# Performance work log

Measured on AMD Instinct MI355X. Metric: run time of the kernel, lower is better.

Reference implementation:

```python
import jax, jax.numpy as jnp
import numpy as np

DIM = 512
HEADS = 8
DHEAD = 64
INNER = HEADS * DHEAD
CHUNK = 8
GAMMA = 1.0
EPS = 1e-8
LN_EPS = 1e-5


def setup_inputs() -> dict:
    key = jax.random.key(0)
    ks = jax.random.split(key, 10)
    B, N = 64, 256
    return {
        "q": jax.random.normal(ks[0], (B, N, DIM), jnp.float32),
        "k": jax.random.normal(ks[1], (B, N, DIM), jnp.float32),
        "v": jax.random.normal(ks[2], (B, N, DIM), jnp.float32),
        "ln_gamma": jnp.ones((DIM,), jnp.float32),
        "ln_beta": jnp.zeros((DIM,), jnp.float32),
        "W_in": jax.random.normal(ks[3], (DIM, INNER), jnp.float32) / np.sqrt(DIM),
        "W_out": jax.random.normal(ks[4], (INNER, DIM), jnp.float32) / np.sqrt(INNER),
        "b_out": jnp.zeros((DIM,), jnp.float32),
        "cov_logit": jnp.asarray(0.6, jnp.float32),
        "var_logit": jnp.asarray(0.2, jnp.float32),
        "use_advanced": 1,
    }


def _layernorm(x, g, b):
    mu = jnp.mean(x, axis=-1, keepdims=True)
    var = jnp.mean(jnp.square(x - mu), axis=-1, keepdims=True)
    return (x - mu) * jax.lax.rsqrt(var + LN_EPS) * g + b


def _transform(t, ln_gamma, ln_beta, W_in):
    # [B,N,dim] -> [h,B,N,d]
    B, N, _ = t.shape
    f = _layernorm(t, ln_gamma, ln_beta) @ W_in
    return f.reshape(B, N, HEADS, DHEAD).transpose(2, 0, 1, 3)


def _chunk_stats(E):
    # E: [M, N, d], chunks of size CHUNK over M. Returns per-chunk scalars V, C of shape [M//CHUNK].
    M, N, d = E.shape
    nc = M // CHUNK
    Ec = E.reshape(nc, CHUNK, N, d)
    # variance component: torch.var is unbiased (ddof=1) over seq dim
    sigma = jnp.sqrt(jnp.var(Ec, axis=2, ddof=1) + EPS)  # [nc, CHUNK, d]
    V = jnp.mean(jax.nn.relu(GAMMA - sigma), axis=(1, 2))  # [nc]
    # covariance component: per-sample off-diagonal energy, averaged per chunk
    centered = Ec - jnp.mean(Ec, axis=2, keepdims=True)
    cov = jnp.einsum("csni,csnj->csij", centered, centered) / (N - 1)  # [nc,CHUNK,d,d]
    total = jnp.sum(jnp.square(cov), axis=(2, 3))
    diag = jnp.sum(jnp.square(jnp.diagonal(cov, axis1=2, axis2=3)), axis=2)
    C = jnp.mean((total - diag) / d, axis=1)  # [nc]
    return V, C


def reference(q, k, v, ln_gamma, ln_beta, W_in, W_out, b_out, cov_logit, var_logit, use_advanced):
    f_q = _transform(q, ln_gamma, ln_beta, W_in)  # [h,B,N,d]
    f_k = _transform(k, ln_gamma, ln_beta, W_in)
    f_v = _transform(v, ln_gamma, ln_beta, W_in)
    h, B, N, d = f_q.shape

    # cosine similarity
    dots_qk = jnp.einsum("hbnd,hbmd->hbnm", f_q, f_k)
    qn = jnp.linalg.norm(f_q, axis=-1)  # [h,B,N]
    kn = jnp.linalg.norm(f_k, axis=-1)
    cosine_sim = dots_qk / (qn[..., :, None] * kn[..., None, :])

    if use_advanced:
        Vq, Cq = _chunk_stats(f_q.reshape(h * B, N, d))
        Vk, Ck = _chunk_stats(f_k.reshape(h * B, N, d))
        var_component = jnp.repeat(Vq * Vk, CHUNK).reshape(h, B, 1, 1)
        cov_component = jnp.repeat(Cq * Ck, CHUNK).reshape(h, B, 1, 1)
    else:
        qc = f_q - jnp.mean(f_q, axis=-1, keepdims=True)
        kc = f_k - jnp.mean(f_k, axis=-1, keepdims=True)
        cov_component = jnp.einsum("hbnd,hbmd->hbnm", qc, kc) / d
        q_var = jnp.var(f_q, axis=-1, ddof=1, keepdims=True)  # [h,B,N,1]
        k_var = jnp.var(f_k, axis=-1, ddof=1, keepdims=True)
        var_component = (q_var * jnp.swapaxes(k_var, -1, -2)) / d

    cov_w = jax.nn.sigmoid(cov_logit)
    var_w = jax.nn.sigmoid(var_logit)
    cos_w = 1.0 - cov_w - var_w
    dots = cos_w * cosine_sim + cov_w * cov_component + var_w * var_component
    out = jnp.einsum("hbnm,hbmd->hbnd", dots, f_v)
    out = out.transpose(1, 2, 0, 3).reshape(B, N, h * d)
    return out @ W_out + b_out
```

## Files before the change

### kernel.cpp

```cpp
#include <hip/hip_runtime.h>
#include <cstdint>
#include <cstddef>

#define DIM    512
#define HEADS  8
#define DHEAD  64
#define NSEQ   256
#define BATCH  64
#define NROWS  (BATCH * NSEQ)
#define HB     (HEADS * BATCH)

typedef unsigned short u16;
typedef __bf16 bf16x8 __attribute__((ext_vector_type(8)));
typedef float  f32x4  __attribute__((ext_vector_type(4)));

__device__ __forceinline__ float sigmoidf_(float x) { return 1.0f / (1.0f + expf(-x)); }

__device__ __forceinline__ u16 f2bf(float f) {
    union { float f; unsigned u; } a; a.f = f;
    return (u16)((a.u + 0x7fffu + ((a.u >> 16) & 1u)) >> 16);
}

__device__ __forceinline__ void gload16(const void* g, void* l) {
    __builtin_amdgcn_global_load_lds((const __attribute__((address_space(1))) void*)g,
                                     (__attribute__((address_space(3))) void*)l, 16, 0, 0);
}

__global__ __launch_bounds__(256)
void transpose_cast_kernel(const float* __restrict__ W0, const float* __restrict__ W1,
                           u16* __restrict__ WT)
{
    __shared__ float tile[64][65];
    const int t = threadIdx.x;
    const int bx = blockIdx.x * 64, by = blockIdx.y * 64;
    const float* W = blockIdx.z ? W1 : W0;
    u16* dst = WT + (size_t)blockIdx.z * 512 * 512;
#pragma unroll
    for (int i = 0; i < 16; ++i) {
        int idx = i * 256 + t, r = idx >> 6, c = idx & 63;
        tile[r][c] = W[(size_t)(by + r) * DIM + bx + c];
    }
    __syncthreads();
#pragma unroll
    for (int i = 0; i < 16; ++i) {
        int idx = i * 256 + t, r = idx >> 6, c = idx & 63;
        dst[(size_t)(bx + r) * DIM + by + c] = f2bf(tile[c][r]);
    }
}

__global__ __launch_bounds__(256)
void ln_cast_kernel(const float* __restrict__ qp, const float* __restrict__ kp,
                    const float* __restrict__ vp, const float* __restrict__ gam,
                    const float* __restrict__ bet, u16* __restrict__ out)
{
    const int wid = threadIdx.x >> 6, lane = threadIdx.x & 63;
    const int row = blockIdx.x * 4 + wid;
    const int tns = row >> 14, lr = row & 16383;
    const float* X = (tns == 0) ? qp : (tns == 1) ? kp : vp;
    const float* xr = X + (size_t)lr * DIM;
    float4 a = *(const float4*)(xr + lane * 8);
    float4 b = *(const float4*)(xr + lane * 8 + 4);
    float v[8] = {a.x, a.y, a.z, a.w, b.x, b.y, b.z, b.w};
    float s = 0.f;
#pragma unroll
    for (int i = 0; i < 8; ++i) s += v[i];
#pragma unroll
    for (int o = 32; o > 0; o >>= 1) s += __shfl_xor(s, o, 64);
    const float mu = s * (1.f / DIM);
    float sq = 0.f;
#pragma unroll
    for (int i = 0; i < 8; ++i) { float d = v[i] - mu; sq += d * d; }
#pragma unroll
    for (int o = 32; o > 0; o >>= 1) sq += __shfl_xor(sq, o, 64);
    const float rstd = rsqrtf(sq * (1.f / DIM) + 1e-5f);
    float4 g0 = *(const float4*)(gam + lane * 8), g1 = *(const float4*)(gam + lane * 8 + 4);
    float4 b0 = *(const float4*)(bet + lane * 8), b1 = *(const float4*)(bet + lane * 8 + 4);
    float gv[8] = {g0.x, g0.y, g0.z, g0.w, g1.x, g1.y, g1.z, g1.w};
    float bv[8] = {b0.x, b0.y, b0.z, b0.w, b1.x, b1.y, b1.z, b1.w};
    union { u16 h[8]; uint4 u; } o16;
#pragma unroll
    for (int i = 0; i < 8; ++i) o16.h[i] = f2bf((v[i] - mu) * rstd * gv[i] + bv[i]);
    *(uint4*)(out + (size_t)row * DIM + lane * 8) = o16.u;
}

__global__ __launch_bounds__(256)
void in_gemm_kernel(const u16* __restrict__ A, const u16* __restrict__ BT,
                    u16* __restrict__ FT, u16* __restrict__ Fseq)
{
    __shared__ u16 shm[128 * 136];
    u16* Ct = shm;
    const int t = threadIdx.x, lane = t & 63, w = t >> 6;
    const int wr = w >> 1, wc = w & 1;
    const int flat = blockIdx.y * 4 + blockIdx.x;
    const int rt = (flat & 7) * 48 + ((flat >> 3) >> 2);
    const int c0 = ((flat >> 3) & 3) * 128;
    const int r0 = rt * 128;
    const int cl = lane & 15, q = lane >> 4;

    f32x4 acc[4][4];
#pragma unroll
    for (int i = 0; i < 4; ++i)
#pragma unroll
        for (int j = 0; j < 4; ++j) acc[i][j] = (f32x4){0.f, 0.f, 0.f, 0.f};

#define STAGE_IN(buf, kk)                                                        \
    {                                                                            \
        _Pragma("unroll")                                                        \
        for (int i = 0; i < 2; ++i) {                                            \
            int idx = i * 256 + t;                                               \
            int row = idx >> 2, ch = idx & 3;                                    \
            gload16(A  + (size_t)(r0 + row) * DIM + (kk) + ch * 8,               \
                    shm + (buf) * 4096 + idx * 8);                               \
            gload16(BT + (size_t)(c0 + row) * DIM + (kk) + ch * 8,               \
                    shm + 8192 + (buf) * 4096 + idx * 8);                        \
        }                                                                        \
    }

#define COMPUTE_IN(buf)                                                          \
    {                                                                            \
        const u16* As = shm + (buf) * 4096;                                      \
        const u16* Bs = shm + 8192 + (buf) * 4096;                               \
        bf16x8 af[4], bfr[4];                                                    \
        _Pragma("unroll")                                                        \
        for (int mi = 0; mi < 4; ++mi)                                           \
            af[mi] = *(const bf16x8*)(As + (wr * 64 + mi * 16 + cl) * 32 + q * 8); \
        _Pragma("unroll")                                                        \
        for (int ni = 0; ni < 4; ++ni)                                           \
            bfr[ni] = *(const bf16x8*)(Bs + (wc * 64 + ni * 16 + cl) * 32 + q * 8); \
        _Pragma("unroll")                                                        \
        for (int mi = 0; mi < 4; ++mi)                                           \
            _Pragma("unroll")                                                    \
            for (int ni = 0; ni < 4; ++ni)                                       \
                acc[mi][ni] = __builtin_amdgcn_mfma_f32_16x16x32_bf16(af[mi],    \
                                  bfr[ni], acc[mi][ni], 0, 0, 0);                \
    }

    STAGE_IN(0, 0);
    __syncthreads();
    for (int k0 = 0; k0 < DIM; k0 += 64) {
        STAGE_IN(1, k0 + 32);
        COMPUTE_IN(0);
        __syncthreads();
        if (k0 + 64 < DIM) STAGE_IN(0, k0 + 64);
        COMPUTE_IN(1);
        __syncthreads();
    }
#undef STAGE_IN
#undef COMPUTE_IN

    const int tns = r0 >> 14, b = (r0 >> 8) & 63, n0 = r0 & 255;
    const int lr0 = r0 & 16383;

    if (tns == 0) {
#pragma unroll
        for (int mi = 0; mi < 4; ++mi) {
            int lrow = wr * 64 + mi * 16 + q * 4;
#pragma unroll
            for (int ni = 0; ni < 4; ++ni) {
                int lcol = wc * 64 + ni * 16 + cl;
#pragma unroll
                for (int r = 0; r < 4; ++r)
                    Ct[(lrow + r) * 136 + lcol] = f2bf(acc[mi][ni][r]);
            }
        }
        __syncthreads();
#pragma unroll
        for (int i = 0; i < 8; ++i) {
            int idx = t + 256 * i, row = idx >> 4, ch = idx & 15;
            *(uint4*)(Fseq + (size_t)(lr0 + row) * DIM + c0 + ch * 8) =
                *(const uint4*)(Ct + row * 136 + ch * 8);
        }
        __syncthreads();
    }
#pragma unroll
    for (int mi = 0; mi < 4; ++mi) {
        int lrow = wr * 64 + mi * 16 + q * 4;
#pragma unroll
        for (int ni = 0; ni < 4; ++ni) {
            int lcol = wc * 64 + ni * 16 + cl;
#pragma unroll
            for (int r = 0; r < 4; ++r)
                Ct[lcol * 136 + lrow + r] = f2bf(acc[mi][ni][r]);
        }
    }
    __syncthreads();
#pragma unroll
    for (int i = 0; i < 8; ++i) {
        int idx = t + 256 * i, lc = idx >> 4, ch = idx & 15;
        *(uint4*)(FT + (((size_t)(tns * 64 + b) * 512 + c0 + lc) * 256 + n0 + ch * 8)) =
            *(const uint4*)(Ct + lc * 136 + ch * 8);
    }
}

__global__ __launch_bounds__(256)
void stats_kernel(const u16* __restrict__ FT, float* __restrict__ norms,
                  float2* __restrict__ vc)
{
    __shared__ u16 ET[64 * 264];
    __shared__ float mu[64];
    __shared__ float red[4][64];
    __shared__ float wr3[4][3];
    const int hb = blockIdx.x, tns = blockIdx.y, h = hb >> 6, b = hb & 63;
    const int t = threadIdx.x, lane = t & 63, w = t >> 6, cl = lane & 15, q = lane >> 4;
    const size_t Fb = ((size_t)(tns * 64 + b) * 512 + h * 64) * 256;

#pragma unroll
    for (int i = 0; i < 8; ++i) {
        int idx = t + 256 * i;
        int row = idx >> 5, ch = idx & 31;
        *(bf16x8*)(ET + row * 264 + ch * 8) =
            *(const bf16x8*)(FT + Fb + (size_t)row * 256 + ch * 8);
    }
    __syncthreads();

    {
        float s = 0.f;
#pragma unroll
        for (int d = 0; d < 64; ++d) {
            float x = (float)*(const __bf16*)(ET + d * 264 + t);
            s += x * x;
        }
        norms[((size_t)tns * HB + hb) * 256 + t] = sqrtf(s);
    }
    {
        int d = t & 63, part = t >> 6;
        float s = 0.f;
#pragma unroll
        for (int i = 0; i < 8; ++i) {
            bf16x8 v8 = *(const bf16x8*)(ET + d * 264 + part * 64 + i * 8);
#pragma unroll
            for (int j = 0; j < 8; ++j) s += (float)v8[j];
        }
        red[part][d] = s;
    }
    __syncthreads();
    if (t < 64) mu[t] = (red[0][t] + red[1][t] + red[2][t] + red[3][t]) * (1.f / 256.f);
    __syncthreads();

    f32x4 g[4];
#pragma unroll
    for (int nj = 0; nj < 4; ++nj) g[nj] = (f32x4){0.f, 0.f, 0.f, 0.f};
#pragma unroll
    for (int ks = 0; ks < 8; ++ks) {
        bf16x8 af = *(const bf16x8*)(ET + (16 * w + cl) * 264 + ks * 32 + q * 8);
#pragma unroll
        for (int nj = 0; nj < 4; ++nj) {
            bf16x8 bfr = *(const bf16x8*)(ET + (16 * nj + cl) * 264 + ks * 32 + q * 8);
            g[nj] = __builtin_amdgcn_mfma_f32_16x16x32_bf16(af, bfr, g[nj], 0, 0, 0);
        }
    }
    float t2 = 0.f, d2 = 0.f, vs = 0.f;
#pragma unroll
    for (int nj = 0; nj < 4; ++nj) {
        int j = 16 * nj + cl;
        float mj = mu[j];
#pragma unroll
        for (int r = 0; r < 4; ++r) {
            int i = 16 * w + 4 * q + r;
            float gc = (g[nj][r] - 256.f * mu[i] * mj) * (1.f / 255.f);
            float g2 = gc * gc;
            t2 += g2;
            if (i == j) {
                d2 += g2;
                float sig = sqrtf(gc + 1e-8f);
                vs += fmaxf(1.f - sig, 0.f);
            }
        }
    }
#pragma unroll
    for (int o = 32; o > 0; o >>= 1) {
        t2 += __shfl_xor(t2, o, 64);
        d2 += __shfl_xor(d2, o, 64);
        vs += __shfl_xor(vs, o, 64);
    }
    if (lane == 0) { wr3[w][0] = t2; wr3[w][1] = d2; wr3[w][2] = vs; }
    __syncthreads();
    if (t == 0) {
        float T = 0.f, D = 0.f, V = 0.f;
        for (int i = 0; i < 4; ++i) { T += wr3[i][0]; D += wr3[i][1]; V += wr3[i][2]; }
        vc[(size_t)tns * HB + hb] = make_float2(V * (1.f / 64.f), (T - D) * (1.f / 64.f));
    }
}

__global__ __launch_bounds__(256)
void attn_kernel(const u16* __restrict__ FT, const u16* __restrict__ Fseq,
                 const float* __restrict__ norms, const float2* __restrict__ vc,
                 const float* __restrict__ cov_logit, const float* __restrict__ var_logit,
                 u16* __restrict__ G)
{
    __shared__ u16 pool[256 * 72];
    __shared__ u16 MT[64 * 72];
    __shared__ float invq[256], invk[256], sv[64];
    const int hb = blockIdx.x, h = hb >> 6, b = hb & 63;
    const int t = threadIdx.x, lane = t & 63, w = t >> 6, cl = lane & 15, q = lane >> 4;
    u16* KT = pool;
    u16* VT = pool + 64 * 136;

    const float cw = sigmoidf_(*cov_logit), vw = sigmoidf_(*var_logit);
    const float cosw = 1.f - cw - vw;
    float s_hb;
    {
        int basec = hb & ~7;
        float vq = 0, cq = 0, vk = 0, ck = 0;
#pragma unroll
        for (int m = 0; m < 8; ++m) {
            float2 a = vc[basec + m];       vq += a.x; cq += a.y;
            float2 bb = vc[HB + basec + m]; vk += bb.x; ck += bb.y;
        }
        s_hb = (cw * cq * ck + vw * vq * vk) * (1.f / 64.f);
    }

    invq[t] = 1.f / norms[((size_t)0 * HB + hb) * 256 + t];
    invk[t] = 1.f / norms[((size_t)1 * HB + hb) * 256 + t];
    __syncthreads();

    const size_t FTk = ((size_t)(1 * 64 + b) * 512 + h * 64) * 256;
    const size_t FTv = ((size_t)(2 * 64 + b) * 512 + h * 64) * 256;
    f32x4 acc1[4];
#pragma unroll
    for (int nj = 0; nj < 4; ++nj) acc1[nj] = (f32x4){0.f, 0.f, 0.f, 0.f};
    float sp[4] = {0.f, 0.f, 0.f, 0.f};

    for (int c = 0; c < 2; ++c) {
#pragma unroll
        for (int i = 0; i < 4; ++i) {
            int idx = t + 256 * i;
            int row = idx >> 4, ch = idx & 15;
            int n0 = c * 128 + ch * 8;
            bf16x8 kv = *(const bf16x8*)(FT + FTk + (size_t)row * 256 + n0);
            bf16x8 vv = *(const bf16x8*)(FT + FTv + (size_t)row * 256 + n0);
            bf16x8 ksc;
#pragma unroll
            for (int j = 0; j < 8; ++j) ksc[j] = (__bf16)((float)kv[j] * invk[n0 + j]);
            *(bf16x8*)(KT + row * 136 + ch * 8) = ksc;
            *(bf16x8*)(VT + row * 136 + ch * 8) = vv;
        }
        __syncthreads();
#pragma unroll
        for (int ks = 0; ks < 4; ++ks) {
            bf16x8 af = *(const bf16x8*)(KT + (16 * w + cl) * 136 + ks * 32 + q * 8);
#pragma unroll
            for (int nj = 0; nj < 4; ++nj) {
                bf16x8 bfr = *(const bf16x8*)(VT + (16 * nj + cl) * 136 + ks * 32 + q * 8);
                if (w == 0) {
                    float s = 0.f;
#pragma unroll
                    for (int j = 0; j < 8; ++j) s += (float)bfr[j];
                    sp[nj] += s;
                }
                acc1[nj] = __builtin_amdgcn_mfma_f32_16x16x32_bf16(af, bfr, acc1[nj], 0, 0, 0);
            }
        }
        __syncthreads();
    }
    if (w == 0) {
#pragma unroll
        for (int nj = 0; nj < 4; ++nj) {
            float s = sp[nj];
            s += __shfl_xor(s, 16, 64);
            s += __shfl_xor(s, 32, 64);
            if (q == 0) sv[16 * nj + cl] = s;
        }
    }
#pragma unroll
    for (int nj = 0; nj < 4; ++nj)
#pragma unroll
        for (int r = 0; r < 4; ++r)
            MT[(16 * nj + cl) * 72 + 16 * w + 4 * q + r] = f2bf(acc1[nj][r]);
    __syncthreads();

    f32x4 acc2[4][4];
#pragma unroll
    for (int mi = 0; mi < 4; ++mi)
#pragma unroll
        for (int nj = 0; nj < 4; ++nj) acc2[mi][nj] = (f32x4){0.f, 0.f, 0.f, 0.f};
    const size_t Fq = (size_t)(b * 256) * DIM + h * 64;
#pragma unroll
    for (int ks2 = 0; ks2 < 2; ++ks2) {
        bf16x8 bfm[4];
#pragma unroll
        for (int nj = 0; nj < 4; ++nj)
            bfm[nj] = *(const bf16x8*)(MT + (16 * nj + cl) * 72 + ks2 * 32 + q * 8);
#pragma unroll
        for (int mi = 0; mi < 4; ++mi) {
            bf16x8 aq = *(const bf16x8*)(Fseq + Fq +
                         (size_t)(64 * w + 16 * mi + cl) * DIM + ks2 * 32 + q * 8);
#pragma unroll
            for (int nj = 0; nj < 4; ++nj)
                acc2[mi][nj] = __builtin_amdgcn_mfma_f32_16x16x32_bf16(aq, bfm[nj],
                                                                       acc2[mi][nj], 0, 0, 0);
        }
    }
    __syncthreads();
    u16* Os = pool;
#pragma unroll
    for (int mi = 0; mi < 4; ++mi) {
        int nbase = 64 * w + 16 * mi + 4 * q;
#pragma unroll
        for (int nj = 0; nj < 4; ++nj) {
            int j = 16 * nj + cl;
            float svj = sv[j];
#pragma unroll
            for (int r = 0; r < 4; ++r) {
                float o = cosw * acc2[mi][nj][r] * invq[nbase + r] + s_hb * svj;
                Os[(nbase + r) * 72 + j] = f2bf(o);
            }
        }
    }
    __syncthreads();
#pragma unroll
    for (int i = 0; i < 8; ++i) {
        int cidx = t + 256 * i;
        int row = cidx >> 3, ch = cidx & 7;
        *(uint4*)(G + (size_t)(b * 256 + row) * DIM + h * 64 + ch * 8) =
            *(const uint4*)(Os + row * 72 + ch * 8);
    }
}

__global__ __launch_bounds__(256)
void out_gemm_kernel(const u16* __restrict__ A, const u16* __restrict__ BT,
                     const float* __restrict__ bias, float* __restrict__ C)
{
    __shared__ u16 As[128 * 32];
    __shared__ u16 Bs[128 * 32];
    const int t = threadIdx.x, lane = t & 63, w = t >> 6;
    const int wr = w >> 1, wc = w & 1;
    const int flat = blockIdx.y * 4 + blockIdx.x;
    const int rt = (flat & 7) * 16 + ((flat >> 3) >> 2);
    const int c0 = ((flat >> 3) & 3) * 128;
    const int r0 = rt * 128;
    const int cl = lane & 15, q = lane >> 4;

    f32x4 acc[4][4];
#pragma unroll
    for (int i = 0; i < 4; ++i)
#pragma unroll
        for (int j = 0; j < 4; ++j) acc[i][j] = (f32x4){0.f, 0.f, 0.f, 0.f};

    for (int k0 = 0; k0 < DIM; k0 += 32) {
#pragma unroll
        for (int i = 0; i < 2; ++i) {
            int idx = i * 256 + t;
            int row = idx >> 2, ch = idx & 3;
            gload16(A  + (size_t)(r0 + row) * DIM + k0 + ch * 8, As + idx * 8);
            gload16(BT + (size_t)(c0 + row) * DIM + k0 + ch * 8, Bs + idx * 8);
        }
        __syncthreads();
        bf16x8 af[4], bfr[4];
#pragma unroll
        for (int mi = 0; mi < 4; ++mi)
            af[mi] = *(const bf16x8*)(As + (wr * 64 + mi * 16 + cl) * 32 + q * 8);
#pragma unroll
        for (int ni = 0; ni < 4; ++ni)
            bfr[ni] = *(const bf16x8*)(Bs + (wc * 64 + ni * 16 + cl) * 32 + q * 8);
#pragma unroll
        for (int mi = 0; mi < 4; ++mi)
#pragma unroll
            for (int ni = 0; ni < 4; ++ni)
                acc[mi][ni] = __builtin_amdgcn_mfma_f32_16x16x32_bf16(af[mi], bfr[ni],
                                                                      acc[mi][ni], 0, 0, 0);
        __syncthreads();
    }
#pragma unroll
    for (int mi = 0; mi < 4; ++mi) {
        int row0 = r0 + wr * 64 + mi * 16 + q * 4;
#pragma unroll
        for (int ni = 0; ni < 4; ++ni) {
            int col = c0 + wc * 64 + ni * 16 + cl;
            float bv = bias[col];
#pragma unroll
            for (int r = 0; r < 4; ++r)
                C[(size_t)(row0 + r) * DIM + col] = acc[mi][ni][r] + bv;
        }
    }
}

extern "C" void kernel_launch(void* const* d_in, const int* in_sizes, int n_in,
                              void* d_out, int out_size, void* d_ws, size_t ws_size,
                              hipStream_t stream)
{
    const float* q         = (const float*)d_in[0];
    const float* k         = (const float*)d_in[1];
    const float* v         = (const float*)d_in[2];
    const float* ln_g      = (const float*)d_in[3];
    const float* ln_b      = (const float*)d_in[4];
    const float* W_in      = (const float*)d_in[5];
    const float* W_out     = (const float*)d_in[6];
    const float* b_out     = (const float*)d_in[7];
    const float* cov_logit = (const float*)d_in[8];
    const float* var_logit = (const float*)d_in[9];
    float* out = (float*)d_out;

    char* base = (char*)d_ws;
    u16*    Abf   = (u16*)base;
    u16*    WT    = (u16*)(base + 50331648);
    u16*    FT    = (u16*)(base + 51380224);
    u16*    Fseq  = (u16*)(base + 101711872);
    float*  norms = (float*)(base + 118489088);
    float2* vc    = (float2*)(base + 119537664);
    u16*    Gb    = Abf;

    transpose_cast_kernel<<<dim3(8, 8, 2), 256, 0, stream>>>(W_in, W_out, WT);
    ln_cast_kernel<<<dim3(3 * NROWS / 4), 256, 0, stream>>>(q, k, v, ln_g, ln_b, Abf);
    in_gemm_kernel<<<dim3(4, 3 * NROWS / 128), 256, 0, stream>>>(Abf, WT, FT, Fseq);
    stats_kernel<<<dim3(HB, 2), 256, 0, stream>>>(FT, norms, vc);
    attn_kernel<<<dim3(HB), 256, 0, stream>>>(FT, Fseq, norms, vc,
                                              cov_logit, var_logit, Gb);
    out_gemm_kernel<<<dim3(4, NROWS / 128), 256, 0, stream>>>(
        Gb, WT + 512 * 512, b_out, out);
}
```

Baseline: 239.2 us.

## Split attention blocks over query halves, alias LDS, double-buffer output GEMM

The attention kernel now launches twice as many blocks, each handling 128 of the 256 query rows. The shared K^T V product is recomputed by both halves. MT and the output staging buffer are aliased into the pool to cut LDS use, which is meant to raise parallelism and occupancy at the cost of duplicated work. The output projection GEMM gains a two-stage LDS double buffer so global-to-LDS loads overlap the MFMA compute of the previous k-slice.

```diff
diff --git a/kernel.cpp b/kernel.cpp
--- a/kernel.cpp
+++ b/kernel.cpp
@@ -288,13 +288,15 @@
                  const float* __restrict__ cov_logit, const float* __restrict__ var_logit,
                  u16* __restrict__ G)
 {
-    __shared__ u16 pool[256 * 72];
-    __shared__ u16 MT[64 * 72];
+    __shared__ u16 pool[64 * 136 * 2];
     __shared__ float invq[256], invk[256], sv[64];
-    const int hb = blockIdx.x, h = hb >> 6, b = hb & 63;
+    const int hb = blockIdx.x & 511, h2 = blockIdx.x >> 9;
+    const int h = hb >> 6, b = hb & 63;
     const int t = threadIdx.x, lane = t & 63, w = t >> 6, cl = lane & 15, q = lane >> 4;
     u16* KT = pool;
     u16* VT = pool + 64 * 136;
+    u16* MT = pool;
+    u16* Os = pool + 4608;
 
     const float cw = sigmoidf_(*cov_logit), vw = sigmoidf_(*var_logit);
     const float cosw = 1.f - cw - vw;
@@ -369,12 +371,12 @@
             MT[(16 * nj + cl) * 72 + 16 * w + 4 * q + r] = f2bf(acc1[nj][r]);
     __syncthreads();
 
-    f32x4 acc2[4][4];
-#pragma unroll
-    for (int mi = 0; mi < 4; ++mi)
+    f32x4 acc2[2][4];
+#pragma unroll
+    for (int mi = 0; mi < 2; ++mi)
 #pragma unroll
         for (int nj = 0; nj < 4; ++nj) acc2[mi][nj] = (f32x4){0.f, 0.f, 0.f, 0.f};
-    const size_t Fq = (size_t)(b * 256) * DIM + h * 64;
+    const size_t Fq = (size_t)(b * 256 + h2 * 128) * DIM + h * 64;
 #pragma unroll
     for (int ks2 = 0; ks2 < 2; ++ks2) {
         bf16x8 bfm[4];
@@ -382,9 +384,9 @@
         for (int nj = 0; nj < 4; ++nj)
             bfm[nj] = *(const bf16x8*)(MT + (16 * nj + cl) * 72 + ks2 * 32 + q * 8);
 #pragma unroll
-        for (int mi = 0; mi < 4; ++mi) {
+        for (int mi = 0; mi < 2; ++mi) {
             bf16x8 aq = *(const bf16x8*)(Fseq + Fq +
-                         (size_t)(64 * w + 16 * mi + cl) * DIM + ks2 * 32 + q * 8);
+                         (size_t)(32 * w + 16 * mi + cl) * DIM + ks2 * 32 + q * 8);
 #pragma unroll
             for (int nj = 0; nj < 4; ++nj)
                 acc2[mi][nj] = __builtin_amdgcn_mfma_f32_16x16x32_bf16(aq, bfm[nj],
@@ -392,27 +394,26 @@
         }
     }
     __syncthreads();
-    u16* Os = pool;
-#pragma unroll
-    for (int mi = 0; mi < 4; ++mi) {
-        int nbase = 64 * w + 16 * mi + 4 * q;
+#pragma unroll
+    for (int mi = 0; mi < 2; ++mi) {
+        int nloc = 32 * w + 16 * mi + 4 * q;
 #pragma unroll
         for (int nj = 0; nj < 4; ++nj) {
             int j = 16 * nj + cl;
             float svj = sv[j];
 #pragma unroll
             for (int r = 0; r < 4; ++r) {
-                float o = cosw * acc2[mi][nj][r] * invq[nbase + r] + s_hb * svj;
-                Os[(nbase + r) * 72 + j] = f2bf(o);
+                float o = cosw * acc2[mi][nj][r] * invq[h2 * 128 + nloc + r] + s_hb * svj;
+                Os[(nloc + r) * 72 + j] = f2bf(o);
             }
         }
     }
     __syncthreads();
 #pragma unroll
-    for (int i = 0; i < 8; ++i) {
+    for (int i = 0; i < 4; ++i) {
         int cidx = t + 256 * i;
         int row = cidx >> 3, ch = cidx & 7;
-        *(uint4*)(G + (size_t)(b * 256 + row) * DIM + h * 64 + ch * 8) =
+        *(uint4*)(G + (size_t)(b * 256 + h2 * 128 + row) * DIM + h * 64 + ch * 8) =
             *(const uint4*)(Os + row * 72 + ch * 8);
     }
 }
@@ -421,8 +422,7 @@
 void out_gemm_kernel(const u16* __restrict__ A, const u16* __restrict__ BT,
                      const float* __restrict__ bias, float* __restrict__ C)
 {
-    __shared__ u16 As[128 * 32];
-    __shared__ u16 Bs[128 * 32];
+    __shared__ u16 shm[16384];
     const int t = threadIdx.x, lane = t & 63, w = t >> 6;
     const int wr = w >> 1, wc = w & 1;
     const int flat = blockIdx.y * 4 + blockIdx.x;
@@ -437,30 +437,51 @@
 #pragma unroll
         for (int j = 0; j < 4; ++j) acc[i][j] = (f32x4){0.f, 0.f, 0.f, 0.f};
 
-    for (int k0 = 0; k0 < DIM; k0 += 32) {
-#pragma unroll
-        for (int i = 0; i < 2; ++i) {
-            int idx = i * 256 + t;
-            int row = idx >> 2, ch = idx & 3;
-            gload16(A  + (size_t)(r0 + row) * DIM + k0 + ch * 8, As + idx * 8);
-            gload16(BT + (size_t)(c0 + row) * DIM + k0 + ch * 8, Bs + idx * 8);
-        }
-        __syncthreads();
-        bf16x8 af[4], bfr[4];
-#pragma unroll
-        for (int mi = 0; mi < 4; ++mi)
-            af[mi] = *(const bf16x8*)(As + (wr * 64 + mi * 16 + cl) * 32 + q * 8);
-#pragma unroll
-        for (int ni = 0; ni < 4; ++ni)
-            bfr[ni] = *(const bf16x8*)(Bs + (wc * 64 + ni * 16 + cl) * 32 + q * 8);
-#pragma unroll
-        for (int mi = 0; mi < 4; ++mi)
-#pragma unroll
-            for (int ni = 0; ni < 4; ++ni)
-                acc[mi][ni] = __builtin_amdgcn_mfma_f32_16x16x32_bf16(af[mi], bfr[ni],
-                                                                      acc[mi][ni], 0, 0, 0);
-        __syncthreads();
-    }
+#define STAGE_OUT(buf, kk)                                                       \
+    {                                                                            \
+        _Pragma("unroll")                                                        \
+        for (int i = 0; i < 2; ++i) {                                            \
+            int idx = i * 256 + t;                                               \
+            int row = idx >> 2, ch = idx & 3;                                    \
+            gload16(A  + (size_t)(r0 + row) * DIM + (kk) + ch * 8,               \
+                    shm + (buf) * 4096 + idx * 8);                               \
+            gload16(BT + (size_t)(c0 + row) * DIM + (kk) + ch * 8,               \
+                    shm + 8192 + (buf) * 4096 + idx * 8);                        \
+        }                                                                        \
+    }
+
+#define COMPUTE_OUT(buf)                                                         \
+    {                                                                            \
+        const u16* As = shm + (buf) * 4096;                                      \
+        const u16* Bs = shm + 8192 + (buf) * 4096;                               \
+        bf16x8 af[4], bfr[4];                                                    \
+        _Pragma("unroll")                                                        \
+        for (int mi = 0; mi < 4; ++mi)                                           \
+            af[mi] = *(const bf16x8*)(As + (wr * 64 + mi * 16 + cl) * 32 + q * 8); \
+        _Pragma("unroll")                                                        \
+        for (int ni = 0; ni < 4; ++ni)                                           \
+            bfr[ni] = *(const bf16x8*)(Bs + (wc * 64 + ni * 16 + cl) * 32 + q * 8); \
+        _Pragma("unroll")                                                        \
+        for (int mi = 0; mi < 4; ++mi)                                           \
+            _Pragma("unroll")                                                    \
+            for (int ni = 0; ni < 4; ++ni)                                       \
+                acc[mi][ni] = __builtin_amdgcn_mfma_f32_16x16x32_bf16(af[mi],    \
+                                  bfr[ni], acc[mi][ni], 0, 0, 0);                \
+    }
+
+    STAGE_OUT(0, 0);
+    __syncthreads();
+    for (int k0 = 0; k0 < DIM; k0 += 64) {
+        STAGE_OUT(1, k0 + 32);
+        COMPUTE_OUT(0);
+        __syncthreads();
+        if (k0 + 64 < DIM) STAGE_OUT(0, k0 + 64);
+        COMPUTE_OUT(1);
+        __syncthreads();
+    }
+#undef STAGE_OUT
+#undef COMPUTE_OUT
+
 #pragma unroll
     for (int mi = 0; mi < 4; ++mi) {
         int row0 = r0 + wr * 64 + mi * 16 + q * 4;
@@ -504,8 +525,8 @@
     ln_cast_kernel<<<dim3(3 * NROWS / 4), 256, 0, stream>>>(q, k, v, ln_g, ln_b, Abf);
     in_gemm_kernel<<<dim3(4, 3 * NROWS / 128), 256, 0, stream>>>(Abf, WT, FT, Fseq);
     stats_kernel<<<dim3(HB, 2), 256, 0, stream>>>(FT, norms, vc);
-    attn_kernel<<<dim3(HB), 256, 0, stream>>>(FT, Fseq, norms, vc,
-                                              cov_logit, var_logit, Gb);
+    attn_kernel<<<dim3(2 * HB), 256, 0, stream>>>(FT, Fseq, norms, vc,
+                                                  cov_logit, var_logit, Gb);
     out_gemm_kernel<<<dim3(4, NROWS / 128), 256, 0, stream>>>(
         Gb, WT + 512 * 512, b_out, out);
 }
```

After: 238.9 us. About the same (-0.1%).
